# Performance work log

Measured on AMD Instinct MI355X. Metric: run time of the kernel, lower is better.

The kernel has to match this reference:

```python
import jax, jax.numpy as jnp
import numpy as np

N, E, F_IN, H, C = 50000, 800000, 256, 128, 40


def _gcn_norm(edge_index, num_nodes, dtype):
    # add self loops (fill value 1.0), symmetric normalization D^-1/2 A D^-1/2
    src, dst = edge_index[0], edge_index[1]
    loop = jnp.arange(num_nodes, dtype=src.dtype)
    src = jnp.concatenate([src, loop])
    dst = jnp.concatenate([dst, loop])
    w = jnp.ones(src.shape[0], dtype=dtype)
    deg = jax.ops.segment_sum(w, dst, num_segments=num_nodes)
    dinv = jnp.where(deg > 0, jax.lax.rsqrt(deg), jnp.zeros_like(deg))
    norm = dinv[src] * w * dinv[dst]
    return src, dst, norm


def _propagate(x, src, dst, w, num_nodes):
    # gather x[src], scale by edge weight, scatter-add at dst (SpMM)
    return jax.ops.segment_sum(w[:, None] * x[src], dst, num_segments=num_nodes)


def _mixhop_conv(x, src, dst, w, Ws, b):
    # powers = [0, 1, 2]; Ws[p] is [in, out]
    n = x.shape[0]
    outs = [x @ Ws[0]]
    h = x
    for p in (1, 2):
        h = _propagate(h, src, dst, w, n)
        outs.append(h @ Ws[p])
    return jnp.concatenate(outs, axis=-1) + b


def setup_inputs() -> dict:
    key = jax.random.key(0)
    ks = jax.random.split(key, 10)
    x = jax.random.normal(ks[0], (N, F_IN), dtype=jnp.float32)
    edge_index = jax.random.randint(ks[1], (2, E), 0, N, dtype=jnp.int64)
    s1 = 1.0 / np.sqrt(F_IN)
    s2 = 1.0 / np.sqrt(3 * H)
    return {
        "x": x,
        "edge_index": edge_index,
        "W1_0": jax.random.uniform(ks[2], (F_IN, H), jnp.float32, -s1, s1),
        "W1_1": jax.random.uniform(ks[3], (F_IN, H), jnp.float32, -s1, s1),
        "W1_2": jax.random.uniform(ks[4], (F_IN, H), jnp.float32, -s1, s1),
        "b1": jnp.zeros((3 * H,), jnp.float32),
        "W2_0": jax.random.uniform(ks[5], (3 * H, C), jnp.float32, -s2, s2),
        "W2_1": jax.random.uniform(ks[6], (3 * H, C), jnp.float32, -s2, s2),
        "W2_2": jax.random.uniform(ks[7], (3 * H, C), jnp.float32, -s2, s2),
        "b2": jnp.zeros((3 * C,), jnp.float32),
    }


def reference(x, edge_index, W1_0, W1_1, W1_2, b1, W2_0, W2_1, W2_2, b2):
    n = x.shape[0]
    src, dst, w = _gcn_norm(edge_index, n, x.dtype)
    h = jax.nn.relu(_mixhop_conv(x, src, dst, w, (W1_0, W1_1, W1_2), b1))
    # eval mode: dropout is identity
    out = _mixhop_conv(h, src, dst, w, (W2_0, W2_1, W2_2), b2)
    return jax.nn.log_softmax(out, axis=1)
```

## Files before the change

### kernel.cpp

```cpp
#include <hip/hip_runtime.h>
#include <hip/hip_bf16.h>
#include <math.h>

#define N_NODES 50000
#define F_IN 256
#define H1 128
#define C_OUT 40
#define L1W 384
#define L2W 120
#define L2WP 128
#define NBUK 196
#define NBLK1 256

typedef __attribute__((ext_vector_type(8))) short short8;
typedef __attribute__((ext_vector_type(4))) float f32x4;
typedef __attribute__((ext_vector_type(2))) float f32x2;

typedef __attribute__((address_space(1))) const unsigned int gu32;
typedef __attribute__((address_space(3))) unsigned int lu32;

__device__ __forceinline__ void g2l16(const void* g, void* l) {
    __builtin_amdgcn_global_load_lds((gu32*)g, (lu32*)l, 16, 0, 0);
}

__device__ inline unsigned short f2bf(float f) {
    union { float f; unsigned int u; } x;
    x.f = f;
    unsigned int u = x.u;
    return (unsigned short)((u + 0x7FFF + ((u >> 16) & 1)) >> 16);
}
__device__ inline float bf2f(unsigned short u) {
    union { unsigned int u; float f; } x;
    x.u = (unsigned int)u << 16;
    return x.f;
}
__device__ inline unsigned int pack_fp8x4(float a, float b, float c, float d) {
    int v = 0;
    v = __builtin_amdgcn_cvt_pk_fp8_f32(a, b, v, false);
    v = __builtin_amdgcn_cvt_pk_fp8_f32(c, d, v, true);
    return (unsigned int)v;
}
__device__ inline unsigned short pack_fp8x2(float a, float b) {
    return (unsigned short)(__builtin_amdgcn_cvt_pk_fp8_f32(a, b, 0, false) & 0xFFFF);
}
__device__ inline unsigned char pack_fp8x1(float a) {
    return (unsigned char)(__builtin_amdgcn_cvt_pk_fp8_f32(a, a, 0, false) & 0xFF);
}
#define EDGE_S(r) ((int)((r) & 0xFFFFu))
#define EDGE_W(r) bf2f((unsigned short)((r) >> 16))


__global__ void detect_k(const int* __restrict__ ei, int* __restrict__ flag) {
    __shared__ int any;
    if (threadIdx.x == 0) any = 0;
    __syncthreads();
    int v = 0;
    for (int r = 0; r < 4; r++) {
        int e = threadIdx.x + r * 256;
        v |= ei[e * 2 + 1];
    }
    if (v != 0) atomicOr(&any, 1);
    __syncthreads();
    if (threadIdx.x == 0) *flag = any;
}


__global__ void hist_k(const int* __restrict__ ei, const int* __restrict__ flag,
                       int* __restrict__ cnt, int E) {
    int base = (blockIdx.x * 256 + threadIdx.x) * 4;
    if (base >= E) return;
    if (base + 4 <= E) {
        int d0, d1, d2, d3;
        if (*flag) {
            int4 dv = *(const int4*)(ei + E + base);
            d0 = dv.x; d1 = dv.y; d2 = dv.z; d3 = dv.w;
        } else {
            const long long* e64 = (const long long*)ei;
            longlong2 a = *(const longlong2*)(e64 + E + base);
            longlong2 b = *(const longlong2*)(e64 + E + base + 2);
            d0 = (int)a.x; d1 = (int)a.y; d2 = (int)b.x; d3 = (int)b.y;
        }
        atomicAdd(&cnt[d0], 1);
        atomicAdd(&cnt[d1], 1);
        atomicAdd(&cnt[d2], 1);
        atomicAdd(&cnt[d3], 1);
    } else {
        for (int e = base; e < E; e++) {
            int d = (*flag) ? ei[E + e] : (int)((const long long*)ei)[E + e];
            atomicAdd(&cnt[d], 1);
        }
    }
}


__global__ __launch_bounds__(256) void scan1_k(const int* __restrict__ cnt,
                                               int* __restrict__ bsum, int n) {
    int t = threadIdx.x;
    int i = blockIdx.x * 256 + t;
    int v = (i < n) ? cnt[i] : 0;
    for (int off = 32; off; off >>= 1) v += __shfl_down(v, off, 64);
    __shared__ int ws[4];
    if ((t & 63) == 0) ws[t >> 6] = v;
    __syncthreads();
    if (t == 0) bsum[blockIdx.x] = ws[0] + ws[1] + ws[2] + ws[3];
}

__global__ __launch_bounds__(256) void scan2_k(int* __restrict__ bsum,
                                               int* __restrict__ btot, int nb) {
    __shared__ int s[256];
    int t = threadIdx.x;
    int v = (t < nb) ? bsum[t] : 0;
    s[t] = v;
    __syncthreads();
    for (int off = 1; off < 256; off <<= 1) {
        int u = (t >= off) ? s[t - off] : 0;
        __syncthreads();
        s[t] += u;
        __syncthreads();
    }
    if (t < nb) bsum[t] = s[t] - v;
    if (t == nb - 1) *btot = s[t];
}

__global__ __launch_bounds__(256) void scan3_k(const int* __restrict__ cnt,
                                               const int* __restrict__ bsum,
                                               int* __restrict__ rowptr,
                                               float* __restrict__ dinv, int n) {
    __shared__ int s[256];
    int t = threadIdx.x;
    int i = blockIdx.x * 256 + t;
    int v = (i < n) ? cnt[i] : 0;
    s[t] = v;
    __syncthreads();
    for (int off = 1; off < 256; off <<= 1) {
        int u = (t >= off) ? s[t - off] : 0;
        __syncthreads();
        s[t] += u;
        __syncthreads();
    }
    if (i < n) {
        rowptr[i] = s[t] - v + bsum[blockIdx.x];
        if (dinv) dinv[i] = rsqrtf((float)v + 1.0f);
    }
}


__global__ __launch_bounds__(256) void hist2_k(const int* __restrict__ ei,
                                               const int* __restrict__ flag,
                                               int* __restrict__ cnt2, int E) {
    __shared__ int lcnt[NBUK];
    int t = threadIdx.x, blk = blockIdx.x;
    for (int j = t; j < NBUK; j += 256) lcnt[j] = 0;
    __syncthreads();
    int chunk = (E + NBLK1 - 1) / NBLK1;
    int beg = blk * chunk, end = min(beg + chunk, E);
    bool i32 = (*flag) != 0;
    const long long* e64 = (const long long*)ei;
    for (int e = beg + t; e < end; e += 256) {
        int d = i32 ? ei[E + e] : (int)e64[E + e];
        atomicAdd(&lcnt[d >> 8], 1);
    }
    __syncthreads();
    for (int j = t; j < NBUK; j += 256) cnt2[j * NBLK1 + blk] = lcnt[j];
}

__global__ __launch_bounds__(256) void stage_k(const int* __restrict__ ei,
                                               const int* __restrict__ flag,
                                               const int* __restrict__ off2,
                                               unsigned int* __restrict__ stage, int E) {
    __shared__ int lcur[NBUK];
    int t = threadIdx.x, blk = blockIdx.x;
    for (int j = t; j < NBUK; j += 256) lcur[j] = off2[j * NBLK1 + blk];
    __syncthreads();
    int chunk = (E + NBLK1 - 1) / NBLK1;
    int beg = blk * chunk, end = min(beg + chunk, E);
    bool i32 = (*flag) != 0;
    const long long* e64 = (const long long*)ei;
    for (int e = beg + t; e < end; e += 256) {
        int s, d;
        if (i32) { s = ei[e]; d = ei[E + e]; }
        else { s = (int)e64[e]; d = (int)e64[E + e]; }
        int b = d >> 8;
        int pos = atomicAdd(&lcur[b], 1);
        stage[pos] = ((unsigned int)(d & 255) << 16) | (unsigned int)s;
    }
}

__global__ __launch_bounds__(256) void scatter2_k(const unsigned int* __restrict__ stage,
                                                  const int* __restrict__ off2,
                                                  const int* __restrict__ rowptr,
                                                  const float* __restrict__ dinv,
                                                  unsigned int* __restrict__ csr,
                                                  int E, int n) {
    __shared__ int lfill[256];
    int b = blockIdx.x, t = threadIdx.x;
    int node0 = b << 8;
    int node = node0 + t;
    lfill[t] = (node < n) ? rowptr[node] : 0;
    __syncthreads();
    int segBeg = off2[b * NBLK1];
    int segEnd = (b == NBUK - 1) ? E : off2[(b + 1) * NBLK1];
    for (int e = segBeg + t; e < segEnd; e += 256) {
        unsigned int rec = stage[e];
        int dl = rec >> 16;
        int s = rec & 0xFFFF;
        int d = node0 + dl;
        float w = dinv[s] * dinv[d];
        int pos = atomicAdd(&lfill[dl], 1);
        csr[pos] = ((unsigned int)f2bf(w) << 16) | (unsigned int)s;
    }
}


#define N1PACK ((F_IN / 32) * L1W * 32)
#define N2PACK ((L1W / 32) * L2WP * 32)

__global__ void pack_k(const float* __restrict__ w10, const float* __restrict__ w11,
                       const float* __restrict__ w12, const float* __restrict__ w20,
                       const float* __restrict__ w21, const float* __restrict__ w22,
                       unsigned short* __restrict__ Bp1, unsigned short* __restrict__ Bp2) {
    int idx = blockIdx.x * 256 + threadIdx.x;
    if (idx < N1PACK) {
        int kt = idx / (L1W * 32);
        int t = idx % (L1W * 32);
        int s = t >> 9;
        int u = t & 511;
        int kq = u >> 7, m = (u >> 3) & 15, kk = u & 7;
        int col = s * 16 + m;
        int k = kt * 32 + kq * 8 + kk;
        int p = col >> 7, c = col & 127;
        const float* w = (p == 0) ? w10 : (p == 1) ? w11 : w12;
        Bp1[idx] = f2bf(w[k * H1 + c]);
    } else if (idx < N1PACK + N2PACK) {
        int j = idx - N1PACK;
        int kt = j / (L2WP * 32);
        int t = j % (L2WP * 32);
        int s = t >> 9;
        int u = t & 511;
        int kq = u >> 7, m = (u >> 3) & 15, kk = u & 7;
        int col = s * 16 + m;
        int k = kt * 32 + kq * 8 + kk;
        unsigned short v = 0;
        if (col < L2W) {
            int p = col / 40, c = col % 40;
            const float* w = (p == 0) ? w20 : (p == 1) ? w21 : w22;
            v = f2bf(w[k * C_OUT + c]);
        }
        Bp2[j] = v;
    }
}


__global__ __launch_bounds__(256, 2) void mgemm1_k(const float* __restrict__ A,
                                                   const unsigned short* __restrict__ Bp,
                                                   const float* __restrict__ b1,
                                                   unsigned short* __restrict__ Hb,
                                                   unsigned char* __restrict__ Y8, int N) {
    __shared__ unsigned short Bls[2][L1W * 32];
    int tid = threadIdx.x;
    int w = tid >> 6, lane = tid & 63;
    int m = lane & 15, kq = lane >> 4;
    int row0 = blockIdx.x * 64 + w * 16;
    int arow = row0 + m;
    if (arow >= N) arow = N - 1;
    const float* Ap = A + (size_t)arow * F_IN + kq * 8;
    const char* srcb = (const char*)Bp + (size_t)(w * 6) * 1024 + (size_t)lane * 16;

    float4 at0[8], at1[8];
#pragma unroll
    for (int kt = 0; kt < 8; kt++) {
        at0[kt] = *(const float4*)(Ap + kt * 32);
        at1[kt] = *(const float4*)(Ap + kt * 32 + 4);
    }
#pragma unroll
    for (int j = 0; j < 6; j++) g2l16(srcb + j * 1024, &Bls[0][(w * 6 + j) * 512]);
#pragma unroll
    for (int j = 0; j < 6; j++) g2l16(srcb + 24576 + j * 1024, &Bls[1][(w * 6 + j) * 512]);
    short8 areg[8];
#pragma unroll
    for (int kt = 0; kt < 8; kt++) {
        float4 u = at0[kt], v = at1[kt];
        short8 a;
        a[0] = (short)f2bf(u.x); a[1] = (short)f2bf(u.y);
        a[2] = (short)f2bf(u.z); a[3] = (short)f2bf(u.w);
        a[4] = (short)f2bf(v.x); a[5] = (short)f2bf(v.y);
        a[6] = (short)f2bf(v.z); a[7] = (short)f2bf(v.w);
        areg[kt] = a;
    }

    f32x4 acc[24];
#pragma unroll
    for (int s = 0; s < 24; s++) acc[s] = (f32x4){0.f, 0.f, 0.f, 0.f};

#pragma unroll
    for (int kt = 0; kt < 8; kt++) {
        if (kt < 7) { asm volatile("s_waitcnt vmcnt(6)" ::: "memory"); }
        else        { asm volatile("s_waitcnt vmcnt(0)" ::: "memory"); }
        __builtin_amdgcn_sched_barrier(0);
        __builtin_amdgcn_s_barrier();
        const unsigned short* Bbuf = Bls[kt & 1];
#pragma unroll
        for (int c = 0; c < 4; c++) {
            short8 bf[6];
#pragma unroll
            for (int j = 0; j < 6; j++)
                bf[j] = *(const short8*)(&Bbuf[(c * 6 + j) * 512 + lane * 8]);
            asm volatile("s_waitcnt lgkmcnt(0)" ::: "memory");
            __builtin_amdgcn_sched_barrier(0);
            if (c == 3) {
                __builtin_amdgcn_s_barrier();
                if (kt < 6) {
#pragma unroll
                    for (int j = 0; j < 6; j++)
                        g2l16(srcb + (size_t)(kt + 2) * 24576 + j * 1024,
                              &Bls[kt & 1][(w * 6 + j) * 512]);
                }
            }
#pragma unroll
            for (int j = 0; j < 6; j++)
                acc[c * 6 + j] = __builtin_amdgcn_mfma_f32_16x16x32_bf16(
                    areg[kt], bf[j], acc[c * 6 + j], 0, 0, 0);
        }
    }

    int crow = row0 + kq * 4;
#pragma unroll
    for (int s = 0; s < 8; s++) {
        int col = s * 16 + m;
        float bias = b1[col];
#pragma unroll
        for (int r2 = 0; r2 < 4; r2++) {
            int row = crow + r2;
            if (row < N) Hb[(size_t)row * L1W + col] = f2bf(fmaxf(acc[s][r2] + bias, 0.f));
        }
    }
#pragma unroll
    for (int r2 = 0; r2 < 4; r2++) {
        int row = crow + r2;
        if (row < N) {
            uint4 u;
            u.x = pack_fp8x4(acc[8][r2], acc[9][r2], acc[10][r2], acc[11][r2]);
            u.y = pack_fp8x4(acc[12][r2], acc[13][r2], acc[14][r2], acc[15][r2]);
            u.z = pack_fp8x4(acc[16][r2], acc[17][r2], acc[18][r2], acc[19][r2]);
            u.w = pack_fp8x4(acc[20][r2], acc[21][r2], acc[22][r2], acc[23][r2]);
            *(uint4*)(Y8 + (size_t)row * 256 + m * 16) = u;
        }
    }
}


__global__ __launch_bounds__(256, 3) void mgemm2_k(const unsigned short* __restrict__ A,
                                                   const unsigned short* __restrict__ Bp,
                                                   unsigned short* __restrict__ Ub,
                                                   unsigned char* __restrict__ U8, int N) {
    __shared__ unsigned short Bls[2][L2WP * 32];
    int tid = threadIdx.x;
    int w = tid >> 6, lane = tid & 63;
    int m = lane & 15, kq = lane >> 4;
    int row0 = blockIdx.x * 64 + w * 16;
    int arow = row0 + m;
    if (arow >= N) arow = N - 1;
    const unsigned short* Ap = A + (size_t)arow * L1W + kq * 8;
    const char* srcb = (const char*)Bp + (size_t)(w * 2) * 1024 + (size_t)lane * 16;

    short8 areg[12];
#pragma unroll
    for (int kt = 0; kt < 12; kt++) areg[kt] = *(const short8*)(Ap + kt * 32);
#pragma unroll
    for (int j = 0; j < 2; j++) g2l16(srcb + j * 1024, &Bls[0][(w * 2 + j) * 512]);
#pragma unroll
    for (int j = 0; j < 2; j++) g2l16(srcb + 8192 + j * 1024, &Bls[1][(w * 2 + j) * 512]);

    f32x4 acc[8];
#pragma unroll
    for (int s = 0; s < 8; s++) acc[s] = (f32x4){0.f, 0.f, 0.f, 0.f};

#pragma unroll
    for (int kt = 0; kt < 12; kt++) {
        if (kt < 11) { asm volatile("s_waitcnt vmcnt(2)" ::: "memory"); }
        else         { asm volatile("s_waitcnt vmcnt(0)" ::: "memory"); }
        __builtin_amdgcn_sched_barrier(0);
        __builtin_amdgcn_s_barrier();
        const unsigned short* Bbuf = Bls[kt & 1];
        short8 bf[8];
#pragma unroll
        for (int j = 0; j < 8; j++)
            bf[j] = *(const short8*)(&Bbuf[j * 512 + lane * 8]);
        asm volatile("s_waitcnt lgkmcnt(0)" ::: "memory");
        __builtin_amdgcn_sched_barrier(0);
        __builtin_amdgcn_s_barrier();
        if (kt < 10) {
#pragma unroll
            for (int j = 0; j < 2; j++)
                g2l16(srcb + (size_t)(kt + 2) * 8192 + j * 1024,
                      &Bls[kt & 1][(w * 2 + j) * 512]);
        }
#pragma unroll
        for (int j = 0; j < 8; j++)
            acc[j] = __builtin_amdgcn_mfma_f32_16x16x32_bf16(areg[kt], bf[j], acc[j], 0, 0, 0);
    }

    int crow = row0 + kq * 4;
#pragma unroll
    for (int s = 0; s < 3; s++) {
        int col = s * 16 + m;
#pragma unroll
        for (int r2 = 0; r2 < 4; r2++) {
            int row = crow + r2;
            if (row < N) Ub[(size_t)row * L2WP + col] = f2bf(acc[s][r2]);
        }
    }
#pragma unroll
    for (int r2 = 0; r2 < 4; r2++) {
        int row = crow + r2;
        if (row < N) {
            uint2 u;
            u.x = pack_fp8x4(acc[0][r2], acc[1][r2], acc[2][r2], acc[3][r2]);
            u.y = pack_fp8x4(acc[4][r2], acc[5][r2], acc[6][r2], acc[7][r2]);
            *(uint2*)(U8 + (size_t)row * 128 + m * 8) = u;
        }
    }
}


__global__ __launch_bounds__(256) void prop256f_k(const unsigned char* __restrict__ Y8,
                                                  unsigned short* __restrict__ Hb,
                                                  unsigned char* __restrict__ T8,
                                                  const int* __restrict__ rowptr,
                                                  const unsigned int* __restrict__ csr,
                                                  const float* __restrict__ dinv,
                                                  const float* __restrict__ b1, int n) {
    int wave = threadIdx.x >> 6, lane = threadIdx.x & 63;
    int i = blockIdx.x * 4 + wave;
    if (i >= n) return;
    int beg = rowptr[i], end = rowptr[i + 1];
    float di = dinv[i];
    const unsigned int* sbase = (const unsigned int*)Y8 + lane;
    unsigned int sv = sbase[(size_t)i * 64];
    float w = di * di;
    f32x2 slo = __builtin_amdgcn_cvt_pk_f32_fp8(sv, false);
    f32x2 shi = __builtin_amdgcn_cvt_pk_f32_fp8(sv, true);
    float a0 = w * slo.x, a1 = w * slo.y, a2 = w * shi.x, a3 = w * shi.y;

#define CONS256(rr, vv)                                                       \
    _Pragma("unroll") for (int e = 0; e < 8; e++) {                           \
        float we = EDGE_W(rr[e]);                                             \
        f32x2 lo = __builtin_amdgcn_cvt_pk_f32_fp8(vv[e], false);             \
        f32x2 hi = __builtin_amdgcn_cvt_pk_f32_fp8(vv[e], true);              \
        a0 = fmaf(we, lo.x, a0);                                              \
        a1 = fmaf(we, lo.y, a1);                                              \
        a2 = fmaf(we, hi.x, a2);                                              \
        a3 = fmaf(we, hi.y, a3);                                              \
    }

    int nfull = (end - beg) >> 3;
    unsigned int rrA[8], rrB[8];
    if (nfull > 0) {
#pragma unroll
        for (int e = 0; e < 8; e++) rrA[e] = csr[beg + e];
        int it = 0;
        while (it + 2 <= nfull) {
            {
                unsigned int vv[8];
#pragma unroll
                for (int e = 0; e < 8; e++) vv[e] = sbase[(size_t)EDGE_S(rrA[e]) * 64];
#pragma unroll
                for (int e = 0; e < 8; e++) rrB[e] = csr[beg + ((it + 1) << 3) + e];
                CONS256(rrA, vv)
            }
            {
                unsigned int vv[8];
#pragma unroll
                for (int e = 0; e < 8; e++) vv[e] = sbase[(size_t)EDGE_S(rrB[e]) * 64];
                if (it + 2 < nfull) {
#pragma unroll
                    for (int e = 0; e < 8; e++) rrA[e] = csr[beg + ((it + 2) << 3) + e];
                }
                CONS256(rrB, vv)
            }
            it += 2;
        }
        if (it < nfull) {
            unsigned int vv[8];
#pragma unroll
            for (int e = 0; e < 8; e++) vv[e] = sbase[(size_t)EDGE_S(rrA[e]) * 64];
            CONS256(rrA, vv)
        }
    }
    int k = beg + (nfull << 3);
    if (k < end) {
        unsigned int rrt[8];
#pragma unroll
        for (int e = 0; e < 8; e++) {
            int idx = k + e;
            rrt[e] = csr[idx < end ? idx : beg];
        }
        unsigned int vv[8];
#pragma unroll
        for (int e = 0; e < 8; e++) vv[e] = sbase[(size_t)EDGE_S(rrt[e]) * 64];
#pragma unroll
        for (int e = 0; e < 8; e++) {
            float we = (k + e < end) ? EDGE_W(rrt[e]) : 0.f;
            f32x2 lo = __builtin_amdgcn_cvt_pk_f32_fp8(vv[e], false);
            f32x2 hi = __builtin_amdgcn_cvt_pk_f32_fp8(vv[e], true);
            a0 = fmaf(we, lo.x, a0);
            a1 = fmaf(we, lo.y, a1);
            a2 = fmaf(we, hi.x, a2);
            a3 = fmaf(we, hi.y, a3);
        }
    }
#undef CONS256
    int m = lane >> 2, jj = lane & 3;
    if (jj < 2) {
        float av[4] = {a0, a1, a2, a3};
#pragma unroll
        for (int j = 0; j < 4; j++) {
            int L = (4 * jj + j) * 16 + m;
            Hb[(size_t)i * L1W + 128 + L] = f2bf(fmaxf(av[j] + b1[128 + L], 0.f));
        }
    } else {
        unsigned int o = pack_fp8x4(a0, a1, a2, a3);
        *(unsigned int*)(T8 + (size_t)i * 128 + m * 8 + 4 * (jj - 2)) = o;
    }
}


__global__ __launch_bounds__(256) void prop128f_k(const unsigned char* __restrict__ T8,
                                                  unsigned short* __restrict__ Hb,
                                                  const int* __restrict__ rowptr,
                                                  const unsigned int* __restrict__ csr,
                                                  const float* __restrict__ dinv,
                                                  const float* __restrict__ b1, int n) {
    int wave = threadIdx.x >> 6, lane = threadIdx.x & 63;
    int i = blockIdx.x * 4 + wave;
    if (i >= n) return;
    int beg = rowptr[i], end = rowptr[i + 1];
    float di = dinv[i];
    const unsigned short* sbase = (const unsigned short*)T8 + lane;
    unsigned int sv = sbase[(size_t)i * 64];
    float w = di * di;
    f32x2 sd = __builtin_amdgcn_cvt_pk_f32_fp8(sv, false);
    float a0 = w * sd.x, a1 = w * sd.y;

#define CONS128(rr, vv)                                                       \
    _Pragma("unroll") for (int e = 0; e < 8; e++) {                           \
        float we = EDGE_W(rr[e]);                                             \
        f32x2 d = __builtin_amdgcn_cvt_pk_f32_fp8(vv[e], false);              \
        a0 = fmaf(we, d.x, a0);                                               \
        a1 = fmaf(we, d.y, a1);                                               \
    }

    int nfull = (end - beg) >> 3;
    unsigned int rrA[8], rrB[8];
    if (nfull > 0) {
#pragma unroll
        for (int e = 0; e < 8; e++) rrA[e] = csr[beg + e];
        int it = 0;
        while (it + 2 <= nfull) {
            {
                unsigned int vv[8];
#pragma unroll
                for (int e = 0; e < 8; e++) vv[e] = sbase[(size_t)EDGE_S(rrA[e]) * 64];
#pragma unroll
                for (int e = 0; e < 8; e++) rrB[e] = csr[beg + ((it + 1) << 3) + e];
                CONS128(rrA, vv)
            }
            {
                unsigned int vv[8];
#pragma unroll
                for (int e = 0; e < 8; e++) vv[e] = sbase[(size_t)EDGE_S(rrB[e]) * 64];
                if (it + 2 < nfull) {
#pragma unroll
                    for (int e = 0; e < 8; e++) rrA[e] = csr[beg + ((it + 2) << 3) + e];
                }
                CONS128(rrB, vv)
            }
            it += 2;
        }
        if (it < nfull) {
            unsigned int vv[8];
#pragma unroll
            for (int e = 0; e < 8; e++) vv[e] = sbase[(size_t)EDGE_S(rrA[e]) * 64];
            CONS128(rrA, vv)
        }
    }
    int k = beg + (nfull << 3);
    if (k < end) {
        unsigned int rrt[8];
#pragma unroll
        for (int e = 0; e < 8; e++) {
            int idx = k + e;
            rrt[e] = csr[idx < end ? idx : beg];
        }
        unsigned int vv[8];
#pragma unroll
        for (int e = 0; e < 8; e++) vv[e] = sbase[(size_t)EDGE_S(rrt[e]) * 64];
#pragma unroll
        for (int e = 0; e < 8; e++) {
            float we = (k + e < end) ? EDGE_W(rrt[e]) : 0.f;
            f32x2 d = __builtin_amdgcn_cvt_pk_f32_fp8(vv[e], false);
            a0 = fmaf(we, d.x, a0);
            a1 = fmaf(we, d.y, a1);
        }
    }
#undef CONS128
    int m = lane >> 2, u0 = (2 * lane) & 7;
    int L0 = u0 * 16 + m, L1 = (u0 + 1) * 16 + m;
    Hb[(size_t)i * L1W + 256 + L0] = f2bf(fmaxf(a0 + b1[256 + L0], 0.f));
    Hb[(size_t)i * L1W + 256 + L1] = f2bf(fmaxf(a1 + b1[256 + L1], 0.f));
}


__global__ __launch_bounds__(256) void propU8_k(const unsigned char* __restrict__ U8,
                                                unsigned short* __restrict__ T2a,
                                                unsigned char* __restrict__ T8b,
                                                const int* __restrict__ rowptr,
                                                const unsigned int* __restrict__ csr,
                                                const float* __restrict__ dinv, int n) {
    int wave = threadIdx.x >> 6, lane = threadIdx.x & 63;
    int i = blockIdx.x * 4 + wave;
    if (i >= n) return;
    int beg = rowptr[i], end = rowptr[i + 1];
    float di = dinv[i];
    int g = lane >> 5, c = lane & 31;
    const unsigned int* sbase = (const unsigned int*)U8 + c;
    float a0 = 0.f, a1 = 0.f, a2 = 0.f, a3 = 0.f;
    if (g == 0) {
        unsigned int sv = sbase[(size_t)i * 32];
        float w = di * di;
        f32x2 lo = __builtin_amdgcn_cvt_pk_f32_fp8(sv, false);
        f32x2 hi = __builtin_amdgcn_cvt_pk_f32_fp8(sv, true);
        a0 = w * lo.x; a1 = w * lo.y; a2 = w * hi.x; a3 = w * hi.y;
    }

#define CONSU8(rr, vv)                                                        \
    _Pragma("unroll") for (int j = 0; j < 4; j++) {                           \
        float we = EDGE_W(rr[j]);                                             \
        f32x2 lo = __builtin_amdgcn_cvt_pk_f32_fp8(vv[j], false);             \
        f32x2 hi = __builtin_amdgcn_cvt_pk_f32_fp8(vv[j], true);              \
        a0 = fmaf(we, lo.x, a0);                                              \
        a1 = fmaf(we, lo.y, a1);                                              \
        a2 = fmaf(we, hi.x, a2);                                              \
        a3 = fmaf(we, hi.y, a3);                                              \
    }

    int k0 = beg + g;
    int cnt = (k0 < end) ? ((end - k0 + 1) >> 1) : 0;
    int nfull = cnt >> 2;
    unsigned int rrA[4], rrB[4];
    if (nfull > 0) {
#pragma unroll
        for (int j = 0; j < 4; j++) rrA[j] = csr[k0 + 2 * j];
        int it = 0;
        while (it + 2 <= nfull) {
            {
                unsigned int vv[4];
#pragma unroll
                for (int j = 0; j < 4; j++) vv[j] = sbase[(size_t)EDGE_S(rrA[j]) * 32];
#pragma unroll
                for (int j = 0; j < 4; j++) rrB[j] = csr[k0 + ((it + 1) << 3) + 2 * j];
                CONSU8(rrA, vv)
            }
            {
                unsigned int vv[4];
#pragma unroll
                for (int j = 0; j < 4; j++) vv[j] = sbase[(size_t)EDGE_S(rrB[j]) * 32];
                if (it + 2 < nfull) {
#pragma unroll
                    for (int j = 0; j < 4; j++) rrA[j] = csr[k0 + ((it + 2) << 3) + 2 * j];
                }
                CONSU8(rrB, vv)
            }
            it += 2;
        }
        if (it < nfull) {
            unsigned int vv[4];
#pragma unroll
            for (int j = 0; j < 4; j++) vv[j] = sbase[(size_t)EDGE_S(rrA[j]) * 32];
            CONSU8(rrA, vv)
        }
    }
    int t0 = nfull << 2;
    if (t0 < cnt) {
        unsigned int rrt[4], vv[4];
#pragma unroll
        for (int j = 0; j < 4; j++) {
            int t = t0 + j;
            rrt[j] = csr[t < cnt ? k0 + 2 * t : beg];
        }
#pragma unroll
        for (int j = 0; j < 4; j++) vv[j] = sbase[(size_t)EDGE_S(rrt[j]) * 32];
#pragma unroll
        for (int j = 0; j < 4; j++) {
            float we = (t0 + j < cnt) ? EDGE_W(rrt[j]) : 0.f;
            f32x2 lo = __builtin_amdgcn_cvt_pk_f32_fp8(vv[j], false);
            f32x2 hi = __builtin_amdgcn_cvt_pk_f32_fp8(vv[j], true);
            a0 = fmaf(we, lo.x, a0);
            a1 = fmaf(we, lo.y, a1);
            a2 = fmaf(we, hi.x, a2);
            a3 = fmaf(we, hi.y, a3);
        }
    }
#undef CONSU8
    a0 += __shfl_xor(a0, 32, 64);
    a1 += __shfl_xor(a1, 32, 64);
    a2 += __shfl_xor(a2, 32, 64);
    a3 += __shfl_xor(a3, 32, 64);
    if (lane < 32) {
        int m = lane >> 1, sb = 4 * (lane & 1);
        float av[4] = {a0, a1, a2, a3};
#pragma unroll
        for (int j = 0; j < 4; j++) {
            int L = (sb + j) * 16 + m;
            if (L >= 40 && L < 80) T2a[(size_t)i * 40 + (L - 40)] = f2bf(av[j]);
            else if (L >= 80 && L < 120) T8b[(size_t)i * 40 + (L - 80)] = pack_fp8x1(av[j]);
        }
    }
}


__global__ __launch_bounds__(256) void lsm_prop_k(const unsigned short* __restrict__ Ub,
                                                  const unsigned short* __restrict__ T2a,
                                                  const unsigned char* __restrict__ T8b,
                                                  const int* __restrict__ rowptr,
                                                  const unsigned int* __restrict__ csr,
                                                  const float* __restrict__ dinv,
                                                  const float* __restrict__ b2,
                                                  float* __restrict__ out, int n) {
    int wave = threadIdx.x >> 6;
    int lane = threadIdx.x & 63;
    int i = blockIdx.x * 4 + wave;
    if (i >= n) return;
    int beg = rowptr[i], end = rowptr[i + 1];
    float di = dinv[i];
    int g = lane / 10;
    int c = lane - g * 10;
    bool act = lane < 60;
    const unsigned int* sb = (const unsigned int*)T8b + c;
    float a0 = 0.f, a1 = 0.f, a2 = 0.f, a3 = 0.f;
    if (lane < 10) {
        unsigned int sv = sb[(size_t)i * 10];
        float w = di * di;
        f32x2 lo = __builtin_amdgcn_cvt_pk_f32_fp8(sv, false);
        f32x2 hi = __builtin_amdgcn_cvt_pk_f32_fp8(sv, true);
        a0 = w * lo.x; a1 = w * lo.y; a2 = w * hi.x; a3 = w * hi.y;
    }

#define CONSLS(rr, vv)                                                        \
    _Pragma("unroll") for (int j = 0; j < 4; j++) {                           \
        float we = EDGE_W(rr[j]);                                             \
        f32x2 lo = __builtin_amdgcn_cvt_pk_f32_fp8(vv[j], false);             \
        f32x2 hi = __builtin_amdgcn_cvt_pk_f32_fp8(vv[j], true);              \
        a0 = fmaf(we, lo.x, a0);                                              \
        a1 = fmaf(we, lo.y, a1);                                              \
        a2 = fmaf(we, hi.x, a2);                                              \
        a3 = fmaf(we, hi.y, a3);                                              \
    }

    int k0 = beg + g;
    int cnt = (act && k0 < end) ? ((end - k0 + 5) / 6) : 0;
    int nfull = cnt >> 2;
    unsigned int rrA[4], rrB[4];
    if (nfull > 0) {
#pragma unroll
        for (int j = 0; j < 4; j++) rrA[j] = csr[k0 + 6 * j];
        int it = 0;
        while (it + 2 <= nfull) {
            {
                unsigned int vv[4];
#pragma unroll
                for (int j = 0; j < 4; j++) vv[j] = sb[(size_t)EDGE_S(rrA[j]) * 10];
#pragma unroll
                for (int j = 0; j < 4; j++) rrB[j] = csr[k0 + (it + 1) * 24 + 6 * j];
                CONSLS(rrA, vv)
            }
            {
                unsigned int vv[4];
#pragma unroll
                for (int j = 0; j < 4; j++) vv[j] = sb[(size_t)EDGE_S(rrB[j]) * 10];
                if (it + 2 < nfull) {
#pragma unroll
                    for (int j = 0; j < 4; j++) rrA[j] = csr[k0 + (it + 2) * 24 + 6 * j];
                }
                CONSLS(rrB, vv)
            }
            it += 2;
        }
        if (it < nfull) {
            unsigned int vv[4];
#pragma unroll
            for (int j = 0; j < 4; j++) vv[j] = sb[(size_t)EDGE_S(rrA[j]) * 10];
            CONSLS(rrA, vv)
        }
    }
    int t0 = nfull << 2;
    if (t0 < cnt) {
        unsigned int rrt[4], vv[4];
#pragma unroll
        for (int j = 0; j < 4; j++) {
            int t = t0 + j;
            rrt[j] = csr[t < cnt ? k0 + 6 * t : beg];
        }
#pragma unroll
        for (int j = 0; j < 4; j++) vv[j] = sb[(size_t)EDGE_S(rrt[j]) * 10];
#pragma unroll
        for (int j = 0; j < 4; j++) {
            float we = (t0 + j < cnt) ? EDGE_W(rrt[j]) : 0.f;
            f32x2 lo = __builtin_amdgcn_cvt_pk_f32_fp8(vv[j], false);
            f32x2 hi = __builtin_amdgcn_cvt_pk_f32_fp8(vv[j], true);
            a0 = fmaf(we, lo.x, a0);
            a1 = fmaf(we, lo.y, a1);
            a2 = fmaf(we, hi.x, a2);
            a3 = fmaf(we, hi.y, a3);
        }
    }
#undef CONSLS
    float r0s = a0, r1s = a1, r2s = a2, r3s = a3;
#pragma unroll
    for (int g2 = 1; g2 < 6; g2++) {
        r0s += __shfl(a0, lane + 10 * g2, 64);
        r1s += __shfl(a1, lane + 10 * g2, 64);
        r2s += __shfl(a2, lane + 10 * g2, 64);
        r3s += __shfl(a3, lane + 10 * g2, 64);
    }
    int j1 = lane + 64;
    int idx = j1 - 80;
    int srcl = (idx < 0) ? 0 : (idx >> 2);
    float s0v = __shfl(r0s, srcl, 64);
    float s1v = __shfl(r1s, srcl, 64);
    float s2v = __shfl(r2s, srcl, 64);
    float s3v = __shfl(r3s, srcl, 64);
    int comp = idx & 3;
    float pv = (comp == 0) ? s0v : (comp == 1) ? s1v : (comp == 2) ? s2v : s3v;
    float v0, v1;
    {
        int j = lane;
        float v = (j >= 40) ? bf2f(T2a[(size_t)i * 40 + (j - 40)]) : bf2f(Ub[(size_t)i * L2WP + j]);
        v0 = v + b2[j];
    }
    if (j1 < 120) {
        float v = (j1 < 80) ? bf2f(T2a[(size_t)i * 40 + (j1 - 40)]) : pv;
        v1 = v + b2[j1];
    } else {
        v1 = -INFINITY;
    }
    float m = fmaxf(v0, v1);
    for (int off = 32; off; off >>= 1) m = fmaxf(m, __shfl_xor(m, off, 64));
    float s = expf(v0 - m) + ((j1 < 120) ? expf(v1 - m) : 0.f);
    for (int off = 32; off; off >>= 1) s += __shfl_xor(s, off, 64);
    float ls = logf(s) + m;
    out[(size_t)i * 120 + lane] = v0 - ls;
    if (j1 < 120) out[(size_t)i * 120 + j1] = v1 - ls;
}


static inline size_t align256(size_t x) { return (x + 255) & ~(size_t)255; }

extern "C" void kernel_launch(void* const* d_in, const int* in_sizes, int n_in,
                              void* d_out, int out_size, void* d_ws, size_t ws_size,
                              hipStream_t stream) {
    const float* x = (const float*)d_in[0];
    const int* ei = (const int*)d_in[1];
    const float* W1_0 = (const float*)d_in[2];
    const float* W1_1 = (const float*)d_in[3];
    const float* W1_2 = (const float*)d_in[4];
    const float* b1 = (const float*)d_in[5];
    const float* W2_0 = (const float*)d_in[6];
    const float* W2_1 = (const float*)d_in[7];
    const float* W2_2 = (const float*)d_in[8];
    const float* b2 = (const float*)d_in[9];
    float* out = (float*)d_out;

    const int n = N_NODES;
    const int E = in_sizes[1] / 2;
    const int nb = (n + 255) / 256;
    const int nbe4 = ((E + 3) / 4 + 255) / 256;
    const int n2 = NBUK * NBLK1;
    const int nb2 = (n2 + 255) / 256;

    char* p = (char*)d_ws;
    size_t off = 0;
    auto alloc = [&](size_t bytes) {
        void* r = p + off;
        off = align256(off + bytes);
        return r;
    };
    int* flag = (int*)alloc(4);
    int* cnt = (int*)alloc((size_t)n * 4);
    int* rowptr = (int*)alloc((size_t)(n + 1) * 4);
    int* bsum = (int*)alloc((size_t)nb * 4);
    float* dinv = (float*)alloc((size_t)n * 4);
    unsigned int* csr = (unsigned int*)alloc((size_t)E * 4);
    int* cnt2 = (int*)alloc((size_t)n2 * 4);
    int* off2 = (int*)alloc((size_t)n2 * 4);
    int* bsum2 = (int*)alloc((size_t)nb2 * 4);
    int* tot2 = (int*)alloc(4);
    unsigned int* stage = (unsigned int*)alloc((size_t)E * 4);
    unsigned short* Bp1 = (unsigned short*)alloc((size_t)N1PACK * 2);
    unsigned short* Bp2 = (unsigned short*)alloc((size_t)N2PACK * 2);
    unsigned short* Hb = (unsigned short*)alloc((size_t)n * L1W * 2);
    unsigned char* Y8 = (unsigned char*)alloc((size_t)n * 256);
    unsigned char* T8 = (unsigned char*)alloc((size_t)n * 128);
    unsigned short* Ub = (unsigned short*)alloc((size_t)n * L2WP * 2);
    unsigned char* U8 = (unsigned char*)alloc((size_t)n * 128);
    unsigned short* T2a = (unsigned short*)alloc((size_t)n * C_OUT * 2);
    unsigned char* T8b = (unsigned char*)alloc((size_t)n * C_OUT);
    (void)ws_size;

    detect_k<<<1, 256, 0, stream>>>(ei, flag);

    hipMemsetAsync(cnt, 0, (size_t)n * 4, stream);
    hist_k<<<nbe4, 256, 0, stream>>>(ei, flag, cnt, E);
    scan1_k<<<nb, 256, 0, stream>>>(cnt, bsum, n);
    scan2_k<<<1, 256, 0, stream>>>(bsum, rowptr + n, nb);
    scan3_k<<<nb, 256, 0, stream>>>(cnt, bsum, rowptr, dinv, n);

    hist2_k<<<NBLK1, 256, 0, stream>>>(ei, flag, cnt2, E);
    scan1_k<<<nb2, 256, 0, stream>>>(cnt2, bsum2, n2);
    scan2_k<<<1, 256, 0, stream>>>(bsum2, tot2, nb2);
    scan3_k<<<nb2, 256, 0, stream>>>(cnt2, bsum2, off2, (float*)nullptr, n2);
    stage_k<<<NBLK1, 256, 0, stream>>>(ei, flag, off2, stage, E);
    scatter2_k<<<NBUK, 256, 0, stream>>>(stage, off2, rowptr, dinv, csr, E, n);

    pack_k<<<(N1PACK + N2PACK + 255) / 256, 256, 0, stream>>>(W1_0, W1_1, W1_2,
                                                              W2_0, W2_1, W2_2, Bp1, Bp2);

    mgemm1_k<<<(n + 63) / 64, 256, 0, stream>>>(x, Bp1, b1, Hb, Y8, n);
    prop256f_k<<<(n + 3) / 4, 256, 0, stream>>>(Y8, Hb, T8, rowptr, csr, dinv, b1, n);
    prop128f_k<<<(n + 3) / 4, 256, 0, stream>>>(T8, Hb, rowptr, csr, dinv, b1, n);

    mgemm2_k<<<(n + 63) / 64, 256, 0, stream>>>(Hb, Bp2, Ub, U8, n);
    propU8_k<<<(n + 3) / 4, 256, 0, stream>>>(U8, T2a, T8b, rowptr, csr, dinv, n);

    lsm_prop_k<<<(n + 3) / 4, 256, 0, stream>>>(Ub, T2a, T8b, rowptr, csr, dinv, b2, out, n);
}
```

Baseline: 344.1 us.

## Fuse graph preprocessing kernels and reschedule MFMA loops in GEMMs

Merges the dtype-detect, both histogram passes and the weight-pack kernel into one launch. It also runs the two scan chains side by side in shared launches, cutting the kernel count roughly in half. Index-width detection is now recomputed per wave with a ballot instead of being read from a flag buffer. In both GEMM kernels, the MFMA issue is moved before the LDS refill barrier and wrapped in s_setprio, aiming to overlap compute with the prefetch. The cost is extra per-block detection loads, and the node histogram atomics now share a pass with the bucket counts.

```diff
diff --git a/kernel.cpp b/kernel.cpp
--- a/kernel.cpp
+++ b/kernel.cpp
@@ -50,63 +50,108 @@
 #define EDGE_W(r) bf2f((unsigned short)((r) >> 16))
 
 
-__global__ void detect_k(const int* __restrict__ ei, int* __restrict__ flag) {
-    __shared__ int any;
-    if (threadIdx.x == 0) any = 0;
-    __syncthreads();
-    int v = 0;
-    for (int r = 0; r < 4; r++) {
-        int e = threadIdx.x + r * 256;
-        v |= ei[e * 2 + 1];
-    }
-    if (v != 0) atomicOr(&any, 1);
-    __syncthreads();
-    if (threadIdx.x == 0) *flag = any;
-}
-
-
-__global__ void hist_k(const int* __restrict__ ei, const int* __restrict__ flag,
-                       int* __restrict__ cnt, int E) {
-    int base = (blockIdx.x * 256 + threadIdx.x) * 4;
-    if (base >= E) return;
-    if (base + 4 <= E) {
-        int d0, d1, d2, d3;
-        if (*flag) {
-            int4 dv = *(const int4*)(ei + E + base);
-            d0 = dv.x; d1 = dv.y; d2 = dv.z; d3 = dv.w;
-        } else {
-            const long long* e64 = (const long long*)ei;
-            longlong2 a = *(const longlong2*)(e64 + E + base);
-            longlong2 b = *(const longlong2*)(e64 + E + base + 2);
-            d0 = (int)a.x; d1 = (int)a.y; d2 = (int)b.x; d3 = (int)b.y;
-        }
-        atomicAdd(&cnt[d0], 1);
-        atomicAdd(&cnt[d1], 1);
-        atomicAdd(&cnt[d2], 1);
-        atomicAdd(&cnt[d3], 1);
+__device__ __forceinline__ bool detect_i32(const int* __restrict__ ei) {
+    int lane = threadIdx.x & 63;
+    int v = ei[2 * lane + 1] | ei[2 * (lane + 64) + 1] |
+            ei[2 * (lane + 128) + 1] | ei[2 * (lane + 192) + 1];
+    return __ballot(v != 0) != 0ULL;
+}
+
+
+#define N1PACK ((F_IN / 32) * L1W * 32)
+#define N2PACK ((L1W / 32) * L2WP * 32)
+#define PACKB ((N1PACK + N2PACK + 255) / 256)
+
+__global__ __launch_bounds__(256) void fhist_k(const int* __restrict__ ei,
+                                               const float* __restrict__ w10,
+                                               const float* __restrict__ w11,
+                                               const float* __restrict__ w12,
+                                               const float* __restrict__ w20,
+                                               const float* __restrict__ w21,
+                                               const float* __restrict__ w22,
+                                               int* __restrict__ cnt,
+                                               int* __restrict__ cnt2,
+                                               unsigned short* __restrict__ Bp1,
+                                               unsigned short* __restrict__ Bp2, int E) {
+    __shared__ int lcnt[NBUK];
+    int t = threadIdx.x, blk = blockIdx.x;
+    if (blk < NBLK1) {
+        bool i32 = detect_i32(ei);
+        for (int j = t; j < NBUK; j += 256) lcnt[j] = 0;
+        __syncthreads();
+        int chunk = (E + NBLK1 - 1) / NBLK1;
+        int beg = blk * chunk, end = min(beg + chunk, E);
+        const long long* e64 = (const long long*)ei;
+        for (int e = beg + t; e < end; e += 256) {
+            int d = i32 ? ei[E + e] : (int)e64[E + e];
+            atomicAdd(&cnt[d], 1);
+            atomicAdd(&lcnt[d >> 8], 1);
+        }
+        __syncthreads();
+        for (int j = t; j < NBUK; j += 256) cnt2[j * NBLK1 + blk] = lcnt[j];
     } else {
-        for (int e = base; e < E; e++) {
-            int d = (*flag) ? ei[E + e] : (int)((const long long*)ei)[E + e];
-            atomicAdd(&cnt[d], 1);
-        }
-    }
-}
-
-
-__global__ __launch_bounds__(256) void scan1_k(const int* __restrict__ cnt,
-                                               int* __restrict__ bsum, int n) {
+        int idx = (blk - NBLK1) * 256 + t;
+        if (idx < N1PACK) {
+            int kt = idx / (L1W * 32);
+            int tt = idx % (L1W * 32);
+            int s = tt >> 9;
+            int u = tt & 511;
+            int kq = u >> 7, m = (u >> 3) & 15, kk = u & 7;
+            int col = s * 16 + m;
+            int k = kt * 32 + kq * 8 + kk;
+            int p = col >> 7, c = col & 127;
+            const float* w = (p == 0) ? w10 : (p == 1) ? w11 : w12;
+            Bp1[idx] = f2bf(w[k * H1 + c]);
+        } else if (idx < N1PACK + N2PACK) {
+            int j = idx - N1PACK;
+            int kt = j / (L2WP * 32);
+            int tt = j % (L2WP * 32);
+            int s = tt >> 9;
+            int u = tt & 511;
+            int kq = u >> 7, m = (u >> 3) & 15, kk = u & 7;
+            int col = s * 16 + m;
+            int k = kt * 32 + kq * 8 + kk;
+            unsigned short v = 0;
+            if (col < L2W) {
+                int p = col / 40, c = col % 40;
+                const float* w = (p == 0) ? w20 : (p == 1) ? w21 : w22;
+                v = f2bf(w[k * C_OUT + c]);
+            }
+            Bp2[j] = v;
+        }
+    }
+}
+
+
+__global__ __launch_bounds__(256) void fscan1_k(const int* __restrict__ cntA,
+                                                int* __restrict__ bsumA, int nA,
+                                                const int* __restrict__ cntB,
+                                                int* __restrict__ bsumB, int nB, int nbA) {
+    int b = blockIdx.x;
+    const int* cnt;
+    int* bsum;
+    int n, bb;
+    if (b < nbA) { cnt = cntA; bsum = bsumA; n = nA; bb = b; }
+    else         { cnt = cntB; bsum = bsumB; n = nB; bb = b - nbA; }
     int t = threadIdx.x;
-    int i = blockIdx.x * 256 + t;
+    int i = bb * 256 + t;
     int v = (i < n) ? cnt[i] : 0;
     for (int off = 32; off; off >>= 1) v += __shfl_down(v, off, 64);
     __shared__ int ws[4];
     if ((t & 63) == 0) ws[t >> 6] = v;
     __syncthreads();
-    if (t == 0) bsum[blockIdx.x] = ws[0] + ws[1] + ws[2] + ws[3];
-}
-
-__global__ __launch_bounds__(256) void scan2_k(int* __restrict__ bsum,
-                                               int* __restrict__ btot, int nb) {
+    if (t == 0) bsum[bb] = ws[0] + ws[1] + ws[2] + ws[3];
+}
+
+__global__ __launch_bounds__(256) void fscan2_k(int* __restrict__ bsumA,
+                                                int* __restrict__ btotA, int nbA,
+                                                int* __restrict__ bsumB,
+                                                int* __restrict__ btotB, int nbB) {
+    int* bsum;
+    int* btot;
+    int nb;
+    if (blockIdx.x == 0) { bsum = bsumA; btot = btotA; nb = nbA; }
+    else                 { bsum = bsumB; btot = btotB; nb = nbB; }
     __shared__ int s[256];
     int t = threadIdx.x;
     int v = (t < nb) ? bsum[t] : 0;
@@ -122,13 +167,24 @@
     if (t == nb - 1) *btot = s[t];
 }
 
-__global__ __launch_bounds__(256) void scan3_k(const int* __restrict__ cnt,
-                                               const int* __restrict__ bsum,
-                                               int* __restrict__ rowptr,
-                                               float* __restrict__ dinv, int n) {
+__global__ __launch_bounds__(256) void fscan3_k(const int* __restrict__ cntA,
+                                                const int* __restrict__ bsumA,
+                                                int* __restrict__ rpA,
+                                                float* __restrict__ dinv, int nA,
+                                                const int* __restrict__ cntB,
+                                                const int* __restrict__ bsumB,
+                                                int* __restrict__ rpB, int nB, int nbA) {
+    int b = blockIdx.x;
+    const int* cnt;
+    const int* bsum;
+    int* rowptr;
+    float* dv;
+    int n, bb;
+    if (b < nbA) { cnt = cntA; bsum = bsumA; rowptr = rpA; dv = dinv; n = nA; bb = b; }
+    else         { cnt = cntB; bsum = bsumB; rowptr = rpB; dv = nullptr; n = nB; bb = b - nbA; }
     __shared__ int s[256];
     int t = threadIdx.x;
-    int i = blockIdx.x * 256 + t;
+    int i = bb * 256 + t;
     int v = (i < n) ? cnt[i] : 0;
     s[t] = v;
     __syncthreads();
@@ -139,42 +195,22 @@
         __syncthreads();
     }
     if (i < n) {
-        rowptr[i] = s[t] - v + bsum[blockIdx.x];
-        if (dinv) dinv[i] = rsqrtf((float)v + 1.0f);
-    }
-}
-
-
-__global__ __launch_bounds__(256) void hist2_k(const int* __restrict__ ei,
-                                               const int* __restrict__ flag,
-                                               int* __restrict__ cnt2, int E) {
-    __shared__ int lcnt[NBUK];
-    int t = threadIdx.x, blk = blockIdx.x;
-    for (int j = t; j < NBUK; j += 256) lcnt[j] = 0;
-    __syncthreads();
-    int chunk = (E + NBLK1 - 1) / NBLK1;
-    int beg = blk * chunk, end = min(beg + chunk, E);
-    bool i32 = (*flag) != 0;
-    const long long* e64 = (const long long*)ei;
-    for (int e = beg + t; e < end; e += 256) {
-        int d = i32 ? ei[E + e] : (int)e64[E + e];
-        atomicAdd(&lcnt[d >> 8], 1);
-    }
-    __syncthreads();
-    for (int j = t; j < NBUK; j += 256) cnt2[j * NBLK1 + blk] = lcnt[j];
-}
+        rowptr[i] = s[t] - v + bsum[bb];
+        if (dv) dv[i] = rsqrtf((float)v + 1.0f);
+    }
+}
+
 
 __global__ __launch_bounds__(256) void stage_k(const int* __restrict__ ei,
-                                               const int* __restrict__ flag,
                                                const int* __restrict__ off2,
                                                unsigned int* __restrict__ stage, int E) {
     __shared__ int lcur[NBUK];
+    bool i32 = detect_i32(ei);
     int t = threadIdx.x, blk = blockIdx.x;
     for (int j = t; j < NBUK; j += 256) lcur[j] = off2[j * NBLK1 + blk];
     __syncthreads();
     int chunk = (E + NBLK1 - 1) / NBLK1;
     int beg = blk * chunk, end = min(beg + chunk, E);
-    bool i32 = (*flag) != 0;
     const long long* e64 = (const long long*)ei;
     for (int e = beg + t; e < end; e += 256) {
         int s, d;
@@ -212,45 +248,6 @@
 }
 
 
-#define N1PACK ((F_IN / 32) * L1W * 32)
-#define N2PACK ((L1W / 32) * L2WP * 32)
-
-__global__ void pack_k(const float* __restrict__ w10, const float* __restrict__ w11,
-                       const float* __restrict__ w12, const float* __restrict__ w20,
-                       const float* __restrict__ w21, const float* __restrict__ w22,
-                       unsigned short* __restrict__ Bp1, unsigned short* __restrict__ Bp2) {
-    int idx = blockIdx.x * 256 + threadIdx.x;
-    if (idx < N1PACK) {
-        int kt = idx / (L1W * 32);
-        int t = idx % (L1W * 32);
-        int s = t >> 9;
-        int u = t & 511;
-        int kq = u >> 7, m = (u >> 3) & 15, kk = u & 7;
-        int col = s * 16 + m;
-        int k = kt * 32 + kq * 8 + kk;
-        int p = col >> 7, c = col & 127;
-        const float* w = (p == 0) ? w10 : (p == 1) ? w11 : w12;
-        Bp1[idx] = f2bf(w[k * H1 + c]);
-    } else if (idx < N1PACK + N2PACK) {
-        int j = idx - N1PACK;
-        int kt = j / (L2WP * 32);
-        int t = j % (L2WP * 32);
-        int s = t >> 9;
-        int u = t & 511;
-        int kq = u >> 7, m = (u >> 3) & 15, kk = u & 7;
-        int col = s * 16 + m;
-        int k = kt * 32 + kq * 8 + kk;
-        unsigned short v = 0;
-        if (col < L2W) {
-            int p = col / 40, c = col % 40;
-            const float* w = (p == 0) ? w20 : (p == 1) ? w21 : w22;
-            v = f2bf(w[k * C_OUT + c]);
-        }
-        Bp2[j] = v;
-    }
-}
-
-
 __global__ __launch_bounds__(256, 2) void mgemm1_k(const float* __restrict__ A,
                                                    const unsigned short* __restrict__ Bp,
                                                    const float* __restrict__ b1,
@@ -296,30 +293,29 @@
     for (int kt = 0; kt < 8; kt++) {
         if (kt < 7) { asm volatile("s_waitcnt vmcnt(6)" ::: "memory"); }
         else        { asm volatile("s_waitcnt vmcnt(0)" ::: "memory"); }
+        __builtin_amdgcn_s_barrier();
         __builtin_amdgcn_sched_barrier(0);
-        __builtin_amdgcn_s_barrier();
         const unsigned short* Bbuf = Bls[kt & 1];
+        __builtin_amdgcn_s_setprio(1);
 #pragma unroll
         for (int c = 0; c < 4; c++) {
             short8 bf[6];
 #pragma unroll
             for (int j = 0; j < 6; j++)
                 bf[j] = *(const short8*)(&Bbuf[(c * 6 + j) * 512 + lane * 8]);
-            asm volatile("s_waitcnt lgkmcnt(0)" ::: "memory");
-            __builtin_amdgcn_sched_barrier(0);
-            if (c == 3) {
-                __builtin_amdgcn_s_barrier();
-                if (kt < 6) {
-#pragma unroll
-                    for (int j = 0; j < 6; j++)
-                        g2l16(srcb + (size_t)(kt + 2) * 24576 + j * 1024,
-                              &Bls[kt & 1][(w * 6 + j) * 512]);
-                }
-            }
 #pragma unroll
             for (int j = 0; j < 6; j++)
                 acc[c * 6 + j] = __builtin_amdgcn_mfma_f32_16x16x32_bf16(
                     areg[kt], bf[j], acc[c * 6 + j], 0, 0, 0);
+        }
+        __builtin_amdgcn_s_setprio(0);
+        asm volatile("s_waitcnt lgkmcnt(0)" ::: "memory");
+        __builtin_amdgcn_s_barrier();
+        if (kt < 6) {
+#pragma unroll
+            for (int j = 0; j < 6; j++)
+                g2l16(srcb + (size_t)(kt + 2) * 24576 + j * 1024,
+                      &Bls[kt & 1][(w * 6 + j) * 512]);
         }
     }
 
@@ -379,15 +375,19 @@
     for (int kt = 0; kt < 12; kt++) {
         if (kt < 11) { asm volatile("s_waitcnt vmcnt(2)" ::: "memory"); }
         else         { asm volatile("s_waitcnt vmcnt(0)" ::: "memory"); }
+        __builtin_amdgcn_s_barrier();
         __builtin_amdgcn_sched_barrier(0);
-        __builtin_amdgcn_s_barrier();
         const unsigned short* Bbuf = Bls[kt & 1];
+        __builtin_amdgcn_s_setprio(1);
         short8 bf[8];
 #pragma unroll
         for (int j = 0; j < 8; j++)
             bf[j] = *(const short8*)(&Bbuf[j * 512 + lane * 8]);
+#pragma unroll
+        for (int j = 0; j < 8; j++)
+            acc[j] = __builtin_amdgcn_mfma_f32_16x16x32_bf16(areg[kt], bf[j], acc[j], 0, 0, 0);
+        __builtin_amdgcn_s_setprio(0);
         asm volatile("s_waitcnt lgkmcnt(0)" ::: "memory");
-        __builtin_amdgcn_sched_barrier(0);
         __builtin_amdgcn_s_barrier();
         if (kt < 10) {
 #pragma unroll
@@ -395,9 +395,6 @@
                 g2l16(srcb + (size_t)(kt + 2) * 8192 + j * 1024,
                       &Bls[kt & 1][(w * 2 + j) * 512]);
         }
-#pragma unroll
-        for (int j = 0; j < 8; j++)
-            acc[j] = __builtin_amdgcn_mfma_f32_16x16x32_bf16(areg[kt], bf[j], acc[j], 0, 0, 0);
     }
 
     int crow = row0 + kq * 4;
@@ -874,7 +871,6 @@
     const int n = N_NODES;
     const int E = in_sizes[1] / 2;
     const int nb = (n + 255) / 256;
-    const int nbe4 = ((E + 3) / 4 + 255) / 256;
     const int n2 = NBUK * NBLK1;
     const int nb2 = (n2 + 255) / 256;
 
@@ -885,7 +881,6 @@
         off = align256(off + bytes);
         return r;
     };
-    int* flag = (int*)alloc(4);
     int* cnt = (int*)alloc((size_t)n * 4);
     int* rowptr = (int*)alloc((size_t)(n + 1) * 4);
     int* bsum = (int*)alloc((size_t)nb * 4);
@@ -907,23 +902,17 @@
     unsigned char* T8b = (unsigned char*)alloc((size_t)n * C_OUT);
     (void)ws_size;
 
-    detect_k<<<1, 256, 0, stream>>>(ei, flag);
-
     hipMemsetAsync(cnt, 0, (size_t)n * 4, stream);
-    hist_k<<<nbe4, 256, 0, stream>>>(ei, flag, cnt, E);
-    scan1_k<<<nb, 256, 0, stream>>>(cnt, bsum, n);
-    scan2_k<<<1, 256, 0, stream>>>(bsum, rowptr + n, nb);
-    scan3_k<<<nb, 256, 0, stream>>>(cnt, bsum, rowptr, dinv, n);
-
-    hist2_k<<<NBLK1, 256, 0, stream>>>(ei, flag, cnt2, E);
-    scan1_k<<<nb2, 256, 0, stream>>>(cnt2, bsum2, n2);
-    scan2_k<<<1, 256, 0, stream>>>(bsum2, tot2, nb2);
-    scan3_k<<<nb2, 256, 0, stream>>>(cnt2, bsum2, off2, (float*)nullptr, n2);
-    stage_k<<<NBLK1, 256, 0, stream>>>(ei, flag, off2, stage, E);
+    fhist_k<<<NBLK1 + PACKB, 256, 0, stream>>>(ei, W1_0, W1_1, W1_2, W2_0, W2_1, W2_2,
+                                               cnt, cnt2, Bp1, Bp2, E);
+
+    fscan1_k<<<nb + nb2, 256, 0, stream>>>(cnt, bsum, n, cnt2, bsum2, n2, nb);
+    fscan2_k<<<2, 256, 0, stream>>>(bsum, rowptr + n, nb, bsum2, tot2, nb2);
+    fscan3_k<<<nb + nb2, 256, 0, stream>>>(cnt, bsum, rowptr, dinv, n,
+                                           cnt2, bsum2, off2, n2, nb);
+
+    stage_k<<<NBLK1, 256, 0, stream>>>(ei, off2, stage, E);
     scatter2_k<<<NBUK, 256, 0, stream>>>(stage, off2, rowptr, dinv, csr, E, n);
-
-    pack_k<<<(N1PACK + N2PACK + 255) / 256, 256, 0, stream>>>(W1_0, W1_1, W1_2,
-                                                              W2_0, W2_1, W2_2, Bp1, Bp2);
 
     mgemm1_k<<<(n + 63) / 64, 256, 0, stream>>>(x, Bp1, b1, Hb, Y8, n);
     prop256f_k<<<(n + 3) / 4, 256, 0, stream>>>(Y8, Hb, T8, rowptr, csr, dinv, b1, n);
```

Result: faster. 327.2 us (-4.9%).
